# Performance work log

Hardware: AMD Instinct MI355X
Metric: run time of the kernel (lower is better)

Reference implementation:

```python
import jax, jax.numpy as jnp
import numpy as np

B, T, D, H, S = 512, 256, 128, 128, 32


def _param(key, shape, scale):
    return (jax.random.normal(key, shape, dtype=jnp.float32) * scale)


def setup_inputs() -> dict:
    key = jax.random.key(0)
    ks = jax.random.split(key, 32)
    sD = 1.0 / np.sqrt(D)
    sH = 1.0 / np.sqrt(H)
    inp = {
        'x': jax.random.normal(ks[0], (B, T, D), dtype=jnp.float32),
        'statics': jax.random.normal(ks[1], (B, S), dtype=jnp.float32),
        'mask': (jax.random.uniform(ks[2], (B, T, D)) > 0.5).astype(jnp.float32),
        'delta': jax.random.uniform(ks[3], (B, T, D), dtype=jnp.float32),
        'x_last_observed': jax.random.normal(ks[4], (B, T, D), dtype=jnp.float32),
        'x_mean': jax.random.normal(ks[5], (B, D), dtype=jnp.float32),
        'hs0': jax.random.normal(ks[6], (B, H), dtype=jnp.float32),
        # GRU-D decay params
        'w_dg_x': _param(ks[7], (D,), sD), 'b_dg_x': jnp.zeros((D,), jnp.float32),
        'W_dg_h': _param(ks[8], (H, D), sD), 'b_dg_h': jnp.zeros((H,), jnp.float32),
        # gates: update z, reset r, candidate h
        'W_z': _param(ks[9], (H, D), sD), 'U_z': _param(ks[10], (H, H), sH),
        'V_z': _param(ks[11], (H, D), sD), 'b_z': jnp.zeros((H,), jnp.float32),
        'W_r': _param(ks[12], (H, D), sD), 'U_r': _param(ks[13], (H, H), sH),
        'V_r': _param(ks[14], (H, D), sD), 'b_r': jnp.zeros((H,), jnp.float32),
        'W_h': _param(ks[15], (H, D), sD), 'U_h': _param(ks[16], (H, H), sH),
        'V_h': _param(ks[17], (H, D), sD), 'b_h': jnp.zeros((H,), jnp.float32),
        # classifier
        'W_out': _param(ks[18], (1, H + S), 1.0 / np.sqrt(H + S)),
        'b_out': jnp.zeros((1,), jnp.float32),
    }
    return inp


def reference(x, statics, mask, delta, x_last_observed, x_mean, hs0,
              w_dg_x, b_dg_x, W_dg_h, b_dg_h,
              W_z, U_z, V_z, b_z, W_r, U_r, V_r, b_r,
              W_h, U_h, V_h, b_h, W_out, b_out):
    # scan over time: inputs [T, B, D]
    xs = jnp.transpose(x, (1, 0, 2))
    ms = jnp.transpose(mask, (1, 0, 2))
    ds = jnp.transpose(delta, (1, 0, 2))
    xl = jnp.transpose(x_last_observed, (1, 0, 2))

    def step(h, inputs):
        xv, m, d, xlast = inputs
        gamma_x = jnp.exp(-jax.nn.relu(w_dg_x * d + b_dg_x))            # [B, D]
        gamma_h = jnp.exp(-jax.nn.relu(d @ W_dg_h.T + b_dg_h))          # [B, H]
        x_hat = m * xv + (1.0 - m) * (gamma_x * xlast + (1.0 - gamma_x) * x_mean)
        h = gamma_h * h
        z = jax.nn.sigmoid(x_hat @ W_z.T + h @ U_z.T + m @ V_z.T + b_z)
        r = jax.nn.sigmoid(x_hat @ W_r.T + h @ U_r.T + m @ V_r.T + b_r)
        h_tilde = jnp.tanh(x_hat @ W_h.T + (r * h) @ U_h.T + m @ V_h.T + b_h)
        h = (1.0 - z) * h + z * h_tilde
        return h, None

    h_final, _ = jax.lax.scan(step, hs0, (xs, ms, ds, xl))
    full = jnp.concatenate([h_final, statics], axis=1)                  # [B, H+S]
    predictions = full @ W_out.T + b_out                                # [B, 1]
    return predictions
```

## Files before the change

kernel.cpp:

```cpp
#include <hip/hip_runtime.h>
#include <stdint.h>


#define B_ 512
#define T_ 256
#define D_ 128
#define H_ 128
#define S_ 32
#define NE 512
#define KA 384
#define M_ (B_*T_)
#define HP 136
#define ESLAB ((size_t)NE * 16)
#define ESTRIDE ((size_t)32 * ESLAB)

typedef __attribute__((ext_vector_type(8))) short short8;
typedef __attribute__((ext_vector_type(4))) float f32x4;

#define BAR_LDS() asm volatile("s_waitcnt lgkmcnt(0)\n\ts_barrier" ::: "memory")

__device__ __forceinline__ unsigned short f2bf(float f) {
  union { float f; uint32_t u; } v; v.f = f;
  return (unsigned short)((v.u + 0x7FFFu + ((v.u >> 16) & 1u)) >> 16);
}
__device__ __forceinline__ unsigned short f2bf_fast(float f) {
  union { float f; uint32_t u; } v; v.f = f;
  return (unsigned short)((v.u + 0x8000u) >> 16);
}
__device__ __forceinline__ float bf2f(uint32_t s) {
  union { uint32_t u; float f; } v; v.u = s << 16;
  return v.f;
}

__device__ __forceinline__ uint2  ldraw(const unsigned short* p) { return *(const uint2*)p; }
__device__ __forceinline__ float4 ldraw(const float* p)          { return *(const float4*)p; }
__device__ __forceinline__ void unp(uint2 v, float o[4]) {
  o[0] = bf2f(v.x & 0xffffu); o[1] = bf2f(v.x >> 16);
  o[2] = bf2f(v.y & 0xffffu); o[3] = bf2f(v.y >> 16);
}
__device__ __forceinline__ void unp(float4 v, float o[4]) {
  o[0] = v.x; o[1] = v.y; o[2] = v.z; o[3] = v.w;
}
__device__ __forceinline__ void st4(unsigned short* p, const float v[4]) {
  uint2 u;
  u.x = (uint32_t)f2bf(v[0]) | ((uint32_t)f2bf(v[1]) << 16);
  u.y = (uint32_t)f2bf(v[2]) | ((uint32_t)f2bf(v[3]) << 16);
  *(uint2*)p = u;
}
__device__ __forceinline__ void st4(float* p, const float v[4]) {
  *(float4*)p = make_float4(v[0], v[1], v[2], v[3]);
}

__device__ __forceinline__ float fsigmoid(float x) {
  return __builtin_amdgcn_rcpf(1.f + __expf(-x));
}
__device__ __forceinline__ float ftanh(float x) {
  return 1.f - 2.f * __builtin_amdgcn_rcpf(1.f + __expf(2.f * x));
}

#define ASYNC_CP16(gsrc, ldst) \
  __builtin_amdgcn_global_load_lds((const __attribute__((address_space(1))) void*)(gsrc), \
                                   (__attribute__((address_space(3))) void*)(ldst), 16, 0, 0)

__global__ void prep_weights(const float* __restrict__ Wz, const float* __restrict__ Vz,
                             const float* __restrict__ Wr, const float* __restrict__ Vr,
                             const float* __restrict__ Wh, const float* __restrict__ Vh,
                             const float* __restrict__ Wdgh,
                             const float* __restrict__ bz, const float* __restrict__ br,
                             const float* __restrict__ bh, const float* __restrict__ bdgh,
                             unsigned short* __restrict__ Wcat, float* __restrict__ bias)
{
  int id = blockIdx.x * 256 + threadIdx.x;
  if (id < NE * KA) {
    int n = id / KA, k = id - n * KA;
    float v = 0.f;
    if (n < 384) {
      int nn = n & 127;
      const float* W = (n < 128) ? Wz : (n < 256) ? Wr : Wh;
      const float* V = (n < 128) ? Vz : (n < 256) ? Vr : Vh;
      if (k < 128)      v = W[nn * 128 + k];
      else if (k < 256) v = V[nn * 128 + (k - 128)];
    } else {
      if (k >= 256) v = Wdgh[(n - 384) * 128 + (k - 256)];
    }
    Wcat[id] = f2bf(v);
  }
  if (id < NE) {
    bias[id] = (id < 128) ? bz[id] : (id < 256) ? br[id - 128]
             : (id < 384) ? bh[id - 256] : bdgh[id - 384];
  }
}

__global__ void build_A(const float* __restrict__ x, const float* __restrict__ mask,
                        const float* __restrict__ delta, const float* __restrict__ xlast,
                        const float* __restrict__ xmean,
                        const float* __restrict__ wdgx, const float* __restrict__ bdgx,
                        unsigned short* __restrict__ Abuf)
{
  int id = blockIdx.x * 256 + threadIdx.x;
  int m = id >> 5;
  int c = id & 31;
  int t = m >> 9;
  int b = m & (B_ - 1);
  int k = c * 4;
  size_t src = ((size_t)b * T_ + t) * D_ + k;
  float4 xv = *(const float4*)(x + src);
  float4 mv = *(const float4*)(mask + src);
  float4 dv = *(const float4*)(delta + src);
  float4 lv = *(const float4*)(xlast + src);
  float4 uv = *(const float4*)(xmean + (size_t)b * D_ + k);
  float4 wv = *(const float4*)(wdgx + k);
  float4 bv = *(const float4*)(bdgx + k);
  const float* xp = (const float*)&xv; const float* mp = (const float*)&mv;
  const float* dp = (const float*)&dv; const float* lp = (const float*)&lv;
  const float* up = (const float*)&uv; const float* wp = (const float*)&wv;
  const float* bp = (const float*)&bv;
  unsigned short xh[4], mm[4], dd[4];
  #pragma unroll
  for (int i = 0; i < 4; ++i) {
    float g = __expf(-fmaxf(wp[i] * dp[i] + bp[i], 0.f));
    float xhat = mp[i] * xp[i] + (1.f - mp[i]) * (g * lp[i] + (1.f - g) * up[i]);
    xh[i] = f2bf(xhat); mm[i] = f2bf(mp[i]); dd[i] = f2bf(dp[i]);
  }
  uint2 px, pm, pd;
  px.x = (uint32_t)xh[0] | ((uint32_t)xh[1] << 16); px.y = (uint32_t)xh[2] | ((uint32_t)xh[3] << 16);
  pm.x = (uint32_t)mm[0] | ((uint32_t)mm[1] << 16); pm.y = (uint32_t)mm[2] | ((uint32_t)mm[3] << 16);
  pd.x = (uint32_t)dd[0] | ((uint32_t)dd[1] << 16); pd.y = (uint32_t)dd[2] | ((uint32_t)dd[3] << 16);
  unsigned short* rowp = Abuf + (size_t)m * KA;
  *(uint2*)(rowp + k)       = px;
  *(uint2*)(rowp + 128 + k) = pm;
  *(uint2*)(rowp + 256 + k) = pd;
}

template <typename ET>
__global__ __launch_bounds__(256, 2) void gemm_phase1(
    const unsigned short* __restrict__ Abuf, const unsigned short* __restrict__ Wcat,
    const float* __restrict__ bias, ET* __restrict__ E)
{
  __shared__ unsigned short As[3][4096];
  __shared__ unsigned short Bs[3][8192];
  const int tid = threadIdx.x;
  const int wave = tid >> 6, lane = tid & 63;
  const int q = lane >> 4, rl = lane & 15;
  const int m0 = blockIdx.x * 128;
  const int n0 = blockIdx.y * 256;
  const int wm = (wave >> 1) * 64, wn = (wave & 1) * 128;

  f32x4 acc[4][8];
  #pragma unroll
  for (int a = 0; a < 4; ++a)
    #pragma unroll
    for (int b = 0; b < 8; ++b) acc[a][b] = (f32x4){0.f, 0.f, 0.f, 0.f};

  #define STAGE(kt_) do {                                                     \
    const int kbase_ = (kt_) * 32; const int buf_ = (kt_) % 3;                \
    _Pragma("unroll")                                                         \
    for (int i = 0; i < 2; ++i) {                                             \
      int chunk = i * 256 + wave * 64 + lane;                                 \
      int row = chunk >> 2, kc = chunk & 3;                                   \
      ASYNC_CP16(Abuf + (size_t)(m0 + row) * KA + kbase_ + kc * 8,            \
                 &As[buf_][(i * 256 + wave * 64) * 8]);                       \
    }                                                                         \
    _Pragma("unroll")                                                         \
    for (int i = 0; i < 4; ++i) {                                             \
      int chunk = i * 256 + wave * 64 + lane;                                 \
      int row = chunk >> 2, kc = chunk & 3;                                   \
      ASYNC_CP16(Wcat + (size_t)(n0 + row) * KA + kbase_ + kc * 8,            \
                 &Bs[buf_][(i * 256 + wave * 64) * 8]);                       \
    }                                                                         \
  } while (0)

  STAGE(0);
  STAGE(1);

  #pragma unroll
  for (int kt = 0; kt < 12; ++kt) {
    if (kt == 11) asm volatile("s_waitcnt vmcnt(0)" ::: "memory");
    else          asm volatile("s_waitcnt vmcnt(6)" ::: "memory");
    asm volatile("s_barrier" ::: "memory");
    if (kt < 10) STAGE(kt + 2);
    const int buf = kt % 3;
    short8 af[4], bfr[8];
    #pragma unroll
    for (int tm = 0; tm < 4; ++tm)
      af[tm] = *(const short8*)(&As[buf][(wm + tm * 16 + rl) * 32 + q * 8]);
    #pragma unroll
    for (int tn = 0; tn < 8; ++tn)
      bfr[tn] = *(const short8*)(&Bs[buf][(wn + tn * 16 + rl) * 32 + q * 8]);
    #pragma unroll
    for (int tm = 0; tm < 4; ++tm)
      #pragma unroll
      for (int tn = 0; tn < 8; ++tn)
        acc[tm][tn] = __builtin_amdgcn_mfma_f32_16x16x32_bf16(af[tm], bfr[tn], acc[tm][tn], 0, 0, 0);
  }
  #undef STAGE

  const int t = m0 >> 9;
  const int bbase = m0 & (B_ - 1);
  #pragma unroll
  for (int tn = 0; tn < 8; ++tn) {
    int n = n0 + wn + tn * 16 + rl;
    float bv = bias[n];
    bool isg = (n >= 384);
    #pragma unroll
    for (int tm = 0; tm < 4; ++tm) {
      int brow = bbase + wm + tm * 16;
      float v[4];
      #pragma unroll
      for (int reg = 0; reg < 4; ++reg) {
        float xv = acc[tm][tn][reg] + bv;
        v[reg] = isg ? __expf(-fmaxf(xv, 0.f)) : xv;
      }
      st4(E + ((size_t)t * 32 + (brow >> 4)) * ESLAB + (size_t)n * 16 + q * 4, v);
    }
  }
}

template <typename ET>
__global__ __launch_bounds__(512, 2) void grud_scan(
    const ET* __restrict__ E,
    const float* __restrict__ Uz, const float* __restrict__ Ur, const float* __restrict__ Uh,
    const float* __restrict__ hs0, const float* __restrict__ statics,
    const float* __restrict__ Wout, const float* __restrict__ bout,
    float* __restrict__ out)
{
  __shared__ unsigned short hdec[16 * HP];
  __shared__ unsigned short rhb[16 * HP];
  __shared__ float hfin[16 * HP];
  const int tid = threadIdx.x;
  const int wave = tid >> 6, lane = tid & 63;
  const int q = lane >> 4, rl = lane & 15;
  const int col = wave * 16 + rl;
  const int b0 = blockIdx.x * 16;

  short8 uz[4], ur[4], uh[4];
  #pragma unroll
  for (int kc = 0; kc < 4; ++kc) {
    int koff = kc * 32 + q * 8;
    const float* pzw = Uz + col * H_ + koff;
    const float* prw = Ur + col * H_ + koff;
    const float* phw = Uh + col * H_ + koff;
    #pragma unroll
    for (int j = 0; j < 8; ++j) {
      uz[kc][j] = (short)f2bf(pzw[j]);
      ur[kc][j] = (short)f2bf(prw[j]);
      uh[kc][j] = (short)f2bf(phw[j]);
    }
  }

  const ET* pz = E + (size_t)blockIdx.x * ESLAB + (size_t)col * 16 + q * 4;
  const ET* pr = pz + 128 * 16;
  const ET* ph = pz + 256 * 16;
  const ET* pg = pz + 384 * 16;

  using RawT = decltype(ldraw((const ET*)nullptr));
  RawT cz, cr, chh, cg, nz{}, nr{}, nh{}, ng{};
  cz  = ldraw(pz);
  cr  = ldraw(pr);
  chh = ldraw(ph);
  cg  = ldraw(pg + ESTRIDE);
  RawT g0raw = ldraw(pg);

  float hd[4], g0[4];
  unp(g0raw, g0);
  #pragma unroll
  for (int reg = 0; reg < 4; ++reg) {
    int row = q * 4 + reg;
    float h0 = hs0[(b0 + row) * H_ + col];
    hd[reg] = g0[reg] * h0;
    hdec[row * HP + col] = f2bf_fast(hd[reg]);
  }
  BAR_LDS();

  for (int t = 0; t < T_; ++t) {
    if (t + 1 < T_) {
      size_t off = (size_t)(t + 1) * ESTRIDE;
      nz = ldraw(pz + off); nr = ldraw(pr + off); nh = ldraw(ph + off);
      if (t + 2 < T_) ng = ldraw(pg + (size_t)(t + 2) * ESTRIDE);
    }
    float Pz[4], Pr[4], Ph[4];
    unp(cz, Pz); unp(cr, Pr); unp(chh, Ph);

    short8 af[4];
    #pragma unroll
    for (int kc = 0; kc < 4; ++kc)
      af[kc] = *(const short8*)(&hdec[rl * HP + kc * 32 + q * 8]);
    f32x4 accz = (f32x4){0.f,0.f,0.f,0.f}, accr = (f32x4){0.f,0.f,0.f,0.f};
    #pragma unroll
    for (int kc = 0; kc < 4; ++kc) {
      accz = __builtin_amdgcn_mfma_f32_16x16x32_bf16(af[kc], uz[kc], accz, 0, 0, 0);
      accr = __builtin_amdgcn_mfma_f32_16x16x32_bf16(af[kc], ur[kc], accr, 0, 0, 0);
    }
    float zz[4];
    #pragma unroll
    for (int reg = 0; reg < 4; ++reg) {
      zz[reg] = fsigmoid(accz[reg] + Pz[reg]);
      float rr = fsigmoid(accr[reg] + Pr[reg]);
      rhb[(q * 4 + reg) * HP + col] = f2bf_fast(rr * hd[reg]);
    }
    BAR_LDS();

    short8 ar[4];
    #pragma unroll
    for (int kc = 0; kc < 4; ++kc)
      ar[kc] = *(const short8*)(&rhb[rl * HP + kc * 32 + q * 8]);
    f32x4 acch = (f32x4){0.f,0.f,0.f,0.f};
    #pragma unroll
    for (int kc = 0; kc < 4; ++kc)
      acch = __builtin_amdgcn_mfma_f32_16x16x32_bf16(ar[kc], uh[kc], acch, 0, 0, 0);

    if (t < T_ - 1) {
      float Gn[4];
      unp(cg, Gn);
      #pragma unroll
      for (int reg = 0; reg < 4; ++reg) {
        float ht = ftanh(acch[reg] + Ph[reg]);
        float hn = hd[reg] + zz[reg] * (ht - hd[reg]);
        hd[reg] = Gn[reg] * hn;
        hdec[(q * 4 + reg) * HP + col] = f2bf_fast(hd[reg]);
      }
    } else {
      #pragma unroll
      for (int reg = 0; reg < 4; ++reg) {
        float ht = ftanh(acch[reg] + Ph[reg]);
        float hn = hd[reg] + zz[reg] * (ht - hd[reg]);
        hfin[(q * 4 + reg) * HP + col] = hn;
      }
    }
    BAR_LDS();

    cz = nz; cr = nr; chh = nh; cg = ng;
  }

  {
    int row = tid >> 5, j = tid & 31;
    float acc = 0.f;
    #pragma unroll
    for (int c0 = 0; c0 < 4; ++c0)
      acc += hfin[row * HP + j + c0 * 32] * Wout[j + c0 * 32];
    acc += statics[(size_t)(b0 + row) * S_ + j] * Wout[H_ + j];
    #pragma unroll
    for (int off = 16; off >= 1; off >>= 1)
      acc += __shfl_down(acc, off, 32);
    if (j == 0) out[b0 + row] = acc + bout[0];
  }
}

template <typename ET>
static void launch_all(void* const* d_in, float* out, char* ws, hipStream_t stream)
{
  const float* x      = (const float*)d_in[0];
  const float* statics= (const float*)d_in[1];
  const float* mask   = (const float*)d_in[2];
  const float* delta  = (const float*)d_in[3];
  const float* xlast  = (const float*)d_in[4];
  const float* xmean  = (const float*)d_in[5];
  const float* hs0    = (const float*)d_in[6];
  const float* wdgx   = (const float*)d_in[7];
  const float* bdgx   = (const float*)d_in[8];
  const float* Wdgh   = (const float*)d_in[9];
  const float* bdgh   = (const float*)d_in[10];
  const float* Wz     = (const float*)d_in[11];
  const float* Uz     = (const float*)d_in[12];
  const float* Vz     = (const float*)d_in[13];
  const float* bz     = (const float*)d_in[14];
  const float* Wr     = (const float*)d_in[15];
  const float* Ur     = (const float*)d_in[16];
  const float* Vr     = (const float*)d_in[17];
  const float* br     = (const float*)d_in[18];
  const float* Wh     = (const float*)d_in[19];
  const float* Uh     = (const float*)d_in[20];
  const float* Vh     = (const float*)d_in[21];
  const float* bh     = (const float*)d_in[22];
  const float* Wout   = (const float*)d_in[23];
  const float* bout   = (const float*)d_in[24];

  const size_t eBytes = (size_t)M_ * NE * sizeof(ET);
  const size_t aBytes = (size_t)M_ * KA * 2;
  const size_t wBytes = (size_t)NE * KA * 2;
  ET* E = (ET*)ws;
  unsigned short* Abuf = (unsigned short*)(ws + eBytes);
  unsigned short* Wcat = (unsigned short*)(ws + eBytes + aBytes);
  float* bias = (float*)(ws + eBytes + aBytes + wBytes);

  prep_weights<<<768, 256, 0, stream>>>(Wz, Vz, Wr, Vr, Wh, Vh, Wdgh,
                                        bz, br, bh, bdgh, Wcat, bias);
  build_A<<<(M_ * 32) / 256, 256, 0, stream>>>(x, mask, delta, xlast, xmean,
                                               wdgx, bdgx, Abuf);
  gemm_phase1<ET><<<dim3(M_ / 128, NE / 256), 256, 0, stream>>>(Abuf, Wcat, bias, E);
  grud_scan<ET><<<B_ / 16, 512, 0, stream>>>(E, Uz, Ur, Uh, hs0, statics, Wout, bout, out);
}

extern "C" void kernel_launch(void* const* d_in, const int* in_sizes, int n_in,
                              void* d_out, int out_size, void* d_ws, size_t ws_size,
                              hipStream_t stream)
{
  char* ws = (char*)d_ws;
  float* out = (float*)d_out;
  const size_t common = (size_t)M_ * KA * 2 + (size_t)NE * KA * 2 + 8192;
  const size_t needF32 = (size_t)M_ * NE * 4 + common;
  const size_t needBF  = (size_t)M_ * NE * 2 + common;
  if (ws_size >= needF32)     launch_all<float>(d_in, out, ws, stream);
  else if (ws_size >= needBF) launch_all<unsigned short>(d_in, out, ws, stream);
}
```

Measured before the change: 574.2 us.

## Fuse input preprocessing into the phase-1 GEMM and widen block to all N

Removes the separate build_A kernel and its bf16 A buffer. The GEMM now loads x, mask, delta and x_last directly, computes x_hat and the bf16 conversion in registers, and writes the result to LDS. Each block now covers all 512 output columns with 512 threads, so the A tile is produced once per M tile instead of once per N split. The cost is that the pipeline drops from three stages to two and waits on vmcnt(0) at every step. The fp32 loads are also synchronous and sit on the critical path, and occupancy falls to one large block per CU.

```diff
diff --git a/kernel.cpp b/kernel.cpp
--- a/kernel.cpp
+++ b/kernel.cpp
@@ -91,60 +91,30 @@
   }
 }
 
-__global__ void build_A(const float* __restrict__ x, const float* __restrict__ mask,
-                        const float* __restrict__ delta, const float* __restrict__ xlast,
-                        const float* __restrict__ xmean,
-                        const float* __restrict__ wdgx, const float* __restrict__ bdgx,
-                        unsigned short* __restrict__ Abuf)
-{
-  int id = blockIdx.x * 256 + threadIdx.x;
-  int m = id >> 5;
-  int c = id & 31;
-  int t = m >> 9;
-  int b = m & (B_ - 1);
-  int k = c * 4;
-  size_t src = ((size_t)b * T_ + t) * D_ + k;
-  float4 xv = *(const float4*)(x + src);
-  float4 mv = *(const float4*)(mask + src);
-  float4 dv = *(const float4*)(delta + src);
-  float4 lv = *(const float4*)(xlast + src);
-  float4 uv = *(const float4*)(xmean + (size_t)b * D_ + k);
-  float4 wv = *(const float4*)(wdgx + k);
-  float4 bv = *(const float4*)(bdgx + k);
-  const float* xp = (const float*)&xv; const float* mp = (const float*)&mv;
-  const float* dp = (const float*)&dv; const float* lp = (const float*)&lv;
-  const float* up = (const float*)&uv; const float* wp = (const float*)&wv;
-  const float* bp = (const float*)&bv;
-  unsigned short xh[4], mm[4], dd[4];
-  #pragma unroll
-  for (int i = 0; i < 4; ++i) {
-    float g = __expf(-fmaxf(wp[i] * dp[i] + bp[i], 0.f));
-    float xhat = mp[i] * xp[i] + (1.f - mp[i]) * (g * lp[i] + (1.f - g) * up[i]);
-    xh[i] = f2bf(xhat); mm[i] = f2bf(mp[i]); dd[i] = f2bf(dp[i]);
-  }
-  uint2 px, pm, pd;
-  px.x = (uint32_t)xh[0] | ((uint32_t)xh[1] << 16); px.y = (uint32_t)xh[2] | ((uint32_t)xh[3] << 16);
-  pm.x = (uint32_t)mm[0] | ((uint32_t)mm[1] << 16); pm.y = (uint32_t)mm[2] | ((uint32_t)mm[3] << 16);
-  pd.x = (uint32_t)dd[0] | ((uint32_t)dd[1] << 16); pd.y = (uint32_t)dd[2] | ((uint32_t)dd[3] << 16);
-  unsigned short* rowp = Abuf + (size_t)m * KA;
-  *(uint2*)(rowp + k)       = px;
-  *(uint2*)(rowp + 128 + k) = pm;
-  *(uint2*)(rowp + 256 + k) = pd;
-}
-
 template <typename ET>
-__global__ __launch_bounds__(256, 2) void gemm_phase1(
-    const unsigned short* __restrict__ Abuf, const unsigned short* __restrict__ Wcat,
+__global__ __launch_bounds__(512, 1) void gemm_fused(
+    const float* __restrict__ x, const float* __restrict__ mask,
+    const float* __restrict__ delta, const float* __restrict__ xlast,
+    const float* __restrict__ xmean,
+    const float* __restrict__ wdgx, const float* __restrict__ bdgx,
+    const unsigned short* __restrict__ Wcat,
     const float* __restrict__ bias, ET* __restrict__ E)
 {
-  __shared__ unsigned short As[3][4096];
-  __shared__ unsigned short Bs[3][8192];
+  __shared__ unsigned short As[2][128 * 32];
+  __shared__ unsigned short Bs[2][512 * 32];
   const int tid = threadIdx.x;
   const int wave = tid >> 6, lane = tid & 63;
   const int q = lane >> 4, rl = lane & 15;
   const int m0 = blockIdx.x * 128;
-  const int n0 = blockIdx.y * 256;
-  const int wm = (wave >> 1) * 64, wn = (wave & 1) * 128;
+  const int t = m0 >> 9;
+  const int bbase = m0 & (B_ - 1);
+  const int wm = (wave >> 2) * 64;
+  const int wn = (wave & 3) * 128;
+
+  const int srow = tid >> 2;
+  const int kq = tid & 3;
+  const int b_g = bbase + srow;
+  const size_t xoff = ((size_t)b_g * T_ + t) * D_;
 
   f32x4 acc[4][8];
   #pragma unroll
@@ -152,54 +122,141 @@
     #pragma unroll
     for (int b = 0; b < 8; ++b) acc[a][b] = (f32x4){0.f, 0.f, 0.f, 0.f};
 
-  #define STAGE(kt_) do {                                                     \
-    const int kbase_ = (kt_) * 32; const int buf_ = (kt_) % 3;                \
-    _Pragma("unroll")                                                         \
-    for (int i = 0; i < 2; ++i) {                                             \
-      int chunk = i * 256 + wave * 64 + lane;                                 \
-      int row = chunk >> 2, kc = chunk & 3;                                   \
-      ASYNC_CP16(Abuf + (size_t)(m0 + row) * KA + kbase_ + kc * 8,            \
-                 &As[buf_][(i * 256 + wave * 64) * 8]);                       \
-    }                                                                         \
+  float4 sx0, sx1, sm0, sm1, sd0, sd1, sl0, sl1;
+
+  #define ISSUE_B(kt_, buf_) do {                                             \
     _Pragma("unroll")                                                         \
     for (int i = 0; i < 4; ++i) {                                             \
-      int chunk = i * 256 + wave * 64 + lane;                                 \
+      int chunk = i * 512 + wave * 64 + lane;                                 \
       int row = chunk >> 2, kc = chunk & 3;                                   \
-      ASYNC_CP16(Wcat + (size_t)(n0 + row) * KA + kbase_ + kc * 8,            \
-                 &Bs[buf_][(i * 256 + wave * 64) * 8]);                       \
+      ASYNC_CP16(Wcat + (size_t)row * KA + (kt_) * 32 + kc * 8,               \
+                 &Bs[buf_][(i * 512 + wave * 64) * 8]);                       \
     }                                                                         \
   } while (0)
 
-  STAGE(0);
-  STAGE(1);
+  #define ISSUE_A(kt_) do {                                                   \
+    if ((kt_) < 4) {                                                          \
+      int d0 = (kt_) * 32 + kq * 8;                                           \
+      sx0 = *(const float4*)(x + xoff + d0);                                  \
+      sx1 = *(const float4*)(x + xoff + d0 + 4);                              \
+      sm0 = *(const float4*)(mask + xoff + d0);                               \
+      sm1 = *(const float4*)(mask + xoff + d0 + 4);                           \
+      sd0 = *(const float4*)(delta + xoff + d0);                              \
+      sd1 = *(const float4*)(delta + xoff + d0 + 4);                          \
+      sl0 = *(const float4*)(xlast + xoff + d0);                              \
+      sl1 = *(const float4*)(xlast + xoff + d0 + 4);                          \
+    } else if ((kt_) < 8) {                                                   \
+      int d0 = ((kt_) - 4) * 32 + kq * 8;                                     \
+      sm0 = *(const float4*)(mask + xoff + d0);                               \
+      sm1 = *(const float4*)(mask + xoff + d0 + 4);                           \
+    } else {                                                                  \
+      int d0 = ((kt_) - 8) * 32 + kq * 8;                                     \
+      sd0 = *(const float4*)(delta + xoff + d0);                              \
+      sd1 = *(const float4*)(delta + xoff + d0 + 4);                          \
+    }                                                                         \
+  } while (0)
+
+  #define CONVERT_A(kt_, buf_) do {                                           \
+    short8 ov;                                                                \
+    if ((kt_) < 4) {                                                          \
+      int d0 = (kt_) * 32 + kq * 8;                                           \
+      float U[8], W[8], C[8], X[8], Mm[8], Dd[8], L[8];                       \
+      *(float4*)&U[0] = *(const float4*)(xmean + (size_t)b_g * D_ + d0);      \
+      *(float4*)&U[4] = *(const float4*)(xmean + (size_t)b_g * D_ + d0 + 4);  \
+      *(float4*)&W[0] = *(const float4*)(wdgx + d0);                          \
+      *(float4*)&W[4] = *(const float4*)(wdgx + d0 + 4);                      \
+      *(float4*)&C[0] = *(const float4*)(bdgx + d0);                          \
+      *(float4*)&C[4] = *(const float4*)(bdgx + d0 + 4);                      \
+      *(float4*)&X[0] = sx0; *(float4*)&X[4] = sx1;                           \
+      *(float4*)&Mm[0] = sm0; *(float4*)&Mm[4] = sm1;                         \
+      *(float4*)&Dd[0] = sd0; *(float4*)&Dd[4] = sd1;                         \
+      *(float4*)&L[0] = sl0; *(float4*)&L[4] = sl1;                           \
+      _Pragma("unroll")                                                       \
+      for (int i = 0; i < 8; ++i) {                                           \
+        float g = __expf(-fmaxf(W[i] * Dd[i] + C[i], 0.f));                   \
+        float xh = Mm[i] * X[i] + (1.f - Mm[i]) * (g * L[i] + (1.f - g) * U[i]); \
+        ov[i] = (short)f2bf(xh);                                              \
+      }                                                                       \
+    } else if ((kt_) < 8) {                                                   \
+      float Mm[8];                                                            \
+      *(float4*)&Mm[0] = sm0; *(float4*)&Mm[4] = sm1;                         \
+      _Pragma("unroll")                                                       \
+      for (int i = 0; i < 8; ++i) ov[i] = (short)f2bf(Mm[i]);                 \
+    } else {                                                                  \
+      float Dd[8];                                                            \
+      *(float4*)&Dd[0] = sd0; *(float4*)&Dd[4] = sd1;                         \
+      _Pragma("unroll")                                                       \
+      for (int i = 0; i < 8; ++i) ov[i] = (short)f2bf(Dd[i]);                 \
+    }                                                                         \
+    *(short8*)(&As[buf_][srow * 32 + kq * 8]) = ov;                           \
+  } while (0)
+
+  ISSUE_A(0); ISSUE_B(0, 0);
+  asm volatile("s_waitcnt vmcnt(0)" ::: "memory");
+  CONVERT_A(0, 0);
+  BAR_LDS();
+  ISSUE_A(1); ISSUE_B(1, 1);
 
   #pragma unroll
   for (int kt = 0; kt < 12; ++kt) {
-    if (kt == 11) asm volatile("s_waitcnt vmcnt(0)" ::: "memory");
-    else          asm volatile("s_waitcnt vmcnt(6)" ::: "memory");
-    asm volatile("s_barrier" ::: "memory");
-    if (kt < 10) STAGE(kt + 2);
-    const int buf = kt % 3;
+    const int cur = kt & 1;
     short8 af[4], bfr[8];
     #pragma unroll
     for (int tm = 0; tm < 4; ++tm)
-      af[tm] = *(const short8*)(&As[buf][(wm + tm * 16 + rl) * 32 + q * 8]);
+      af[tm] = *(const short8*)(&As[cur][(wm + tm * 16 + rl) * 32 + q * 8]);
     #pragma unroll
     for (int tn = 0; tn < 8; ++tn)
-      bfr[tn] = *(const short8*)(&Bs[buf][(wn + tn * 16 + rl) * 32 + q * 8]);
+      bfr[tn] = *(const short8*)(&Bs[cur][(wn + tn * 16 + rl) * 32 + q * 8]);
     #pragma unroll
     for (int tm = 0; tm < 4; ++tm)
       #pragma unroll
       for (int tn = 0; tn < 8; ++tn)
         acc[tm][tn] = __builtin_amdgcn_mfma_f32_16x16x32_bf16(af[tm], bfr[tn], acc[tm][tn], 0, 0, 0);
-  }
-  #undef STAGE
-
-  const int t = m0 >> 9;
-  const int bbase = m0 & (B_ - 1);
+    if (kt < 11) {
+      asm volatile("s_waitcnt vmcnt(0)" ::: "memory");
+      if (kt == 0)      CONVERT_A(1, 1);
+      else if (kt == 1) CONVERT_A(2, 0);
+      else if (kt == 2) CONVERT_A(3, 1);
+      else if (kt == 3) CONVERT_A(4, 0);
+      else if (kt == 4) CONVERT_A(5, 1);
+      else if (kt == 5) CONVERT_A(6, 0);
+      else if (kt == 6) CONVERT_A(7, 1);
+      else if (kt == 7) CONVERT_A(8, 0);
+      else if (kt == 8) CONVERT_A(9, 1);
+      else if (kt == 9) CONVERT_A(10, 0);
+      else              CONVERT_A(11, 1);
+      BAR_LDS();
+      if (kt < 10) {
+        if (kt == 0)      { ISSUE_A(2); }
+        else if (kt == 1) { ISSUE_A(3); }
+        else if (kt == 2) { ISSUE_A(4); }
+        else if (kt == 3) { ISSUE_A(5); }
+        else if (kt == 4) { ISSUE_A(6); }
+        else if (kt == 5) { ISSUE_A(7); }
+        else if (kt == 6) { ISSUE_A(8); }
+        else if (kt == 7) { ISSUE_A(9); }
+        else if (kt == 8) { ISSUE_A(10); }
+        else              { ISSUE_A(11); }
+        if (kt == 0)      ISSUE_B(2, 0);
+        else if (kt == 1) ISSUE_B(3, 1);
+        else if (kt == 2) ISSUE_B(4, 0);
+        else if (kt == 3) ISSUE_B(5, 1);
+        else if (kt == 4) ISSUE_B(6, 0);
+        else if (kt == 5) ISSUE_B(7, 1);
+        else if (kt == 6) ISSUE_B(8, 0);
+        else if (kt == 7) ISSUE_B(9, 1);
+        else if (kt == 8) ISSUE_B(10, 0);
+        else              ISSUE_B(11, 1);
+      }
+    }
+  }
+  #undef ISSUE_A
+  #undef ISSUE_B
+  #undef CONVERT_A
+
   #pragma unroll
   for (int tn = 0; tn < 8; ++tn) {
-    int n = n0 + wn + tn * 16 + rl;
+    int n = wn + tn * 16 + rl;
     float bv = bias[n];
     bool isg = (n >= 384);
     #pragma unroll
@@ -376,18 +433,15 @@
   const float* bout   = (const float*)d_in[24];
 
   const size_t eBytes = (size_t)M_ * NE * sizeof(ET);
-  const size_t aBytes = (size_t)M_ * KA * 2;
   const size_t wBytes = (size_t)NE * KA * 2;
   ET* E = (ET*)ws;
-  unsigned short* Abuf = (unsigned short*)(ws + eBytes);
-  unsigned short* Wcat = (unsigned short*)(ws + eBytes + aBytes);
-  float* bias = (float*)(ws + eBytes + aBytes + wBytes);
+  unsigned short* Wcat = (unsigned short*)(ws + eBytes);
+  float* bias = (float*)(ws + eBytes + wBytes);
 
   prep_weights<<<768, 256, 0, stream>>>(Wz, Vz, Wr, Vr, Wh, Vh, Wdgh,
                                         bz, br, bh, bdgh, Wcat, bias);
-  build_A<<<(M_ * 32) / 256, 256, 0, stream>>>(x, mask, delta, xlast, xmean,
-                                               wdgx, bdgx, Abuf);
-  gemm_phase1<ET><<<dim3(M_ / 128, NE / 256), 256, 0, stream>>>(Abuf, Wcat, bias, E);
+  gemm_fused<ET><<<M_ / 128, 512, 0, stream>>>(x, mask, delta, xlast, xmean,
+                                               wdgx, bdgx, Wcat, bias, E);
   grud_scan<ET><<<B_ / 16, 512, 0, stream>>>(E, Uz, Ur, Uh, hs0, statics, Wout, bout, out);
 }
 
@@ -397,7 +451,7 @@
 {
   char* ws = (char*)d_ws;
   float* out = (float*)d_out;
-  const size_t common = (size_t)M_ * KA * 2 + (size_t)NE * KA * 2 + 8192;
+  const size_t common = (size_t)NE * KA * 2 + 8192;
   const size_t needF32 = (size_t)M_ * NE * 4 + common;
   const size_t needBF  = (size_t)M_ * NE * 2 + common;
   if (ws_size >= needF32)     launch_all<float>(d_in, out, ws, stream);
```

Measured after the change: 681.6 us. 1.19x slower.

## Always store gate pre-activations in bf16 and restructure build_A per batch row

Applied to the files above, without the earlier changes.

Drops the fp32 intermediate path, so the big E buffer of gate pre-activations is always written and read as bf16, halving its memory traffic between the GEMM and the scan. build_A now runs one block per batch row and loops over time, reading the inputs contiguously and writing Abuf with nontemporal stores. The bf16 intermediate adds rounding error to the recurrence compared with the fp32 path, which was previously chosen whenever the workspace was large enough.

```diff
diff --git a/kernel.cpp b/kernel.cpp
--- a/kernel.cpp
+++ b/kernel.cpp
@@ -32,23 +32,16 @@
   return v.f;
 }
 
-__device__ __forceinline__ uint2  ldraw(const unsigned short* p) { return *(const uint2*)p; }
-__device__ __forceinline__ float4 ldraw(const float* p)          { return *(const float4*)p; }
+__device__ __forceinline__ uint2 ldraw(const unsigned short* p) { return *(const uint2*)p; }
 __device__ __forceinline__ void unp(uint2 v, float o[4]) {
   o[0] = bf2f(v.x & 0xffffu); o[1] = bf2f(v.x >> 16);
   o[2] = bf2f(v.y & 0xffffu); o[3] = bf2f(v.y >> 16);
-}
-__device__ __forceinline__ void unp(float4 v, float o[4]) {
-  o[0] = v.x; o[1] = v.y; o[2] = v.z; o[3] = v.w;
 }
 __device__ __forceinline__ void st4(unsigned short* p, const float v[4]) {
   uint2 u;
   u.x = (uint32_t)f2bf(v[0]) | ((uint32_t)f2bf(v[1]) << 16);
   u.y = (uint32_t)f2bf(v[2]) | ((uint32_t)f2bf(v[3]) << 16);
   *(uint2*)p = u;
-}
-__device__ __forceinline__ void st4(float* p, const float v[4]) {
-  *(float4*)p = make_float4(v[0], v[1], v[2], v[3]);
 }
 
 __device__ __forceinline__ float fsigmoid(float x) {
@@ -91,51 +84,56 @@
   }
 }
 
-__global__ void build_A(const float* __restrict__ x, const float* __restrict__ mask,
-                        const float* __restrict__ delta, const float* __restrict__ xlast,
-                        const float* __restrict__ xmean,
-                        const float* __restrict__ wdgx, const float* __restrict__ bdgx,
-                        unsigned short* __restrict__ Abuf)
-{
-  int id = blockIdx.x * 256 + threadIdx.x;
-  int m = id >> 5;
-  int c = id & 31;
-  int t = m >> 9;
-  int b = m & (B_ - 1);
-  int k = c * 4;
-  size_t src = ((size_t)b * T_ + t) * D_ + k;
-  float4 xv = *(const float4*)(x + src);
-  float4 mv = *(const float4*)(mask + src);
-  float4 dv = *(const float4*)(delta + src);
-  float4 lv = *(const float4*)(xlast + src);
-  float4 uv = *(const float4*)(xmean + (size_t)b * D_ + k);
-  float4 wv = *(const float4*)(wdgx + k);
-  float4 bv = *(const float4*)(bdgx + k);
-  const float* xp = (const float*)&xv; const float* mp = (const float*)&mv;
-  const float* dp = (const float*)&dv; const float* lp = (const float*)&lv;
-  const float* up = (const float*)&uv; const float* wp = (const float*)&wv;
-  const float* bp = (const float*)&bv;
-  unsigned short xh[4], mm[4], dd[4];
-  #pragma unroll
-  for (int i = 0; i < 4; ++i) {
-    float g = __expf(-fmaxf(wp[i] * dp[i] + bp[i], 0.f));
-    float xhat = mp[i] * xp[i] + (1.f - mp[i]) * (g * lp[i] + (1.f - g) * up[i]);
-    xh[i] = f2bf(xhat); mm[i] = f2bf(mp[i]); dd[i] = f2bf(dp[i]);
-  }
-  uint2 px, pm, pd;
-  px.x = (uint32_t)xh[0] | ((uint32_t)xh[1] << 16); px.y = (uint32_t)xh[2] | ((uint32_t)xh[3] << 16);
-  pm.x = (uint32_t)mm[0] | ((uint32_t)mm[1] << 16); pm.y = (uint32_t)mm[2] | ((uint32_t)mm[3] << 16);
-  pd.x = (uint32_t)dd[0] | ((uint32_t)dd[1] << 16); pd.y = (uint32_t)dd[2] | ((uint32_t)dd[3] << 16);
-  unsigned short* rowp = Abuf + (size_t)m * KA;
-  *(uint2*)(rowp + k)       = px;
-  *(uint2*)(rowp + 128 + k) = pm;
-  *(uint2*)(rowp + 256 + k) = pd;
-}
-
-template <typename ET>
+__global__ __launch_bounds__(256, 4) void build_A(
+    const float* __restrict__ x, const float* __restrict__ mask,
+    const float* __restrict__ delta, const float* __restrict__ xlast,
+    const float* __restrict__ xmean,
+    const float* __restrict__ wdgx, const float* __restrict__ bdgx,
+    unsigned short* __restrict__ Abuf)
+{
+  const int b = blockIdx.x;
+  const int dq = (threadIdx.x & 31) * 4;
+  const int tof = threadIdx.x >> 5;
+  const float4 wv = *(const float4*)(wdgx + dq);
+  const float4 cv = *(const float4*)(bdgx + dq);
+  const float4 uv = *(const float4*)(xmean + (size_t)b * D_ + dq);
+  const float* wp = (const float*)&wv;
+  const float* cp = (const float*)&cv;
+  const float* up = (const float*)&uv;
+  const size_t base = (size_t)b * T_ * D_;
+
+  for (int it = 0; it < T_ / 8; ++it) {
+    const int t = it * 8 + tof;
+    const size_t src = base + (size_t)t * D_ + dq;
+    float4 xv = *(const float4*)(x + src);
+    float4 mv = *(const float4*)(mask + src);
+    float4 dv = *(const float4*)(delta + src);
+    float4 lv = *(const float4*)(xlast + src);
+    const float* xp = (const float*)&xv; const float* mp = (const float*)&mv;
+    const float* dp = (const float*)&dv; const float* lp = (const float*)&lv;
+    unsigned short xh[4], mm[4], dd[4];
+    #pragma unroll
+    for (int i = 0; i < 4; ++i) {
+      float g = __expf(-fmaxf(wp[i] * dp[i] + cp[i], 0.f));
+      float xhat = mp[i] * xp[i] + (1.f - mp[i]) * (g * lp[i] + (1.f - g) * up[i]);
+      xh[i] = f2bf(xhat); mm[i] = f2bf(mp[i]); dd[i] = f2bf(dp[i]);
+    }
+    unsigned long long px = (unsigned long long)xh[0] | ((unsigned long long)xh[1] << 16)
+                          | ((unsigned long long)xh[2] << 32) | ((unsigned long long)xh[3] << 48);
+    unsigned long long pm = (unsigned long long)mm[0] | ((unsigned long long)mm[1] << 16)
+                          | ((unsigned long long)mm[2] << 32) | ((unsigned long long)mm[3] << 48);
+    unsigned long long pd = (unsigned long long)dd[0] | ((unsigned long long)dd[1] << 16)
+                          | ((unsigned long long)dd[2] << 32) | ((unsigned long long)dd[3] << 48);
+    unsigned short* rowp = Abuf + (size_t)(t * B_ + b) * KA;
+    __builtin_nontemporal_store(px, (unsigned long long*)(rowp + dq));
+    __builtin_nontemporal_store(pm, (unsigned long long*)(rowp + 128 + dq));
+    __builtin_nontemporal_store(pd, (unsigned long long*)(rowp + 256 + dq));
+  }
+}
+
 __global__ __launch_bounds__(256, 2) void gemm_phase1(
     const unsigned short* __restrict__ Abuf, const unsigned short* __restrict__ Wcat,
-    const float* __restrict__ bias, ET* __restrict__ E)
+    const float* __restrict__ bias, unsigned short* __restrict__ E)
 {
   __shared__ unsigned short As[3][4096];
   __shared__ unsigned short Bs[3][8192];
@@ -216,9 +214,8 @@
   }
 }
 
-template <typename ET>
 __global__ __launch_bounds__(512, 2) void grud_scan(
-    const ET* __restrict__ E,
+    const unsigned short* __restrict__ E,
     const float* __restrict__ Uz, const float* __restrict__ Ur, const float* __restrict__ Uh,
     const float* __restrict__ hs0, const float* __restrict__ statics,
     const float* __restrict__ Wout, const float* __restrict__ bout,
@@ -248,18 +245,17 @@
     }
   }
 
-  const ET* pz = E + (size_t)blockIdx.x * ESLAB + (size_t)col * 16 + q * 4;
-  const ET* pr = pz + 128 * 16;
-  const ET* ph = pz + 256 * 16;
-  const ET* pg = pz + 384 * 16;
-
-  using RawT = decltype(ldraw((const ET*)nullptr));
-  RawT cz, cr, chh, cg, nz{}, nr{}, nh{}, ng{};
+  const unsigned short* pz = E + (size_t)blockIdx.x * ESLAB + (size_t)col * 16 + q * 4;
+  const unsigned short* pr = pz + 128 * 16;
+  const unsigned short* ph = pz + 256 * 16;
+  const unsigned short* pg = pz + 384 * 16;
+
+  uint2 cz, cr, chh, cg, nz{}, nr{}, nh{}, ng{};
   cz  = ldraw(pz);
   cr  = ldraw(pr);
   chh = ldraw(ph);
   cg  = ldraw(pg + ESTRIDE);
-  RawT g0raw = ldraw(pg);
+  uint2 g0raw = ldraw(pg);
 
   float hd[4], g0[4];
   unp(g0raw, g0);
@@ -346,7 +342,6 @@
   }
 }
 
-template <typename ET>
 static void launch_all(void* const* d_in, float* out, char* ws, hipStream_t stream)
 {
   const float* x      = (const float*)d_in[0];
@@ -375,20 +370,20 @@
   const float* Wout   = (const float*)d_in[23];
   const float* bout   = (const float*)d_in[24];
 
-  const size_t eBytes = (size_t)M_ * NE * sizeof(ET);
+  const size_t eBytes = (size_t)M_ * NE * 2;
   const size_t aBytes = (size_t)M_ * KA * 2;
   const size_t wBytes = (size_t)NE * KA * 2;
-  ET* E = (ET*)ws;
+  unsigned short* E = (unsigned short*)ws;
   unsigned short* Abuf = (unsigned short*)(ws + eBytes);
   unsigned short* Wcat = (unsigned short*)(ws + eBytes + aBytes);
   float* bias = (float*)(ws + eBytes + aBytes + wBytes);
 
   prep_weights<<<768, 256, 0, stream>>>(Wz, Vz, Wr, Vr, Wh, Vh, Wdgh,
                                         bz, br, bh, bdgh, Wcat, bias);
-  build_A<<<(M_ * 32) / 256, 256, 0, stream>>>(x, mask, delta, xlast, xmean,
-                                               wdgx, bdgx, Abuf);
-  gemm_phase1<ET><<<dim3(M_ / 128, NE / 256), 256, 0, stream>>>(Abuf, Wcat, bias, E);
-  grud_scan<ET><<<B_ / 16, 512, 0, stream>>>(E, Uz, Ur, Uh, hs0, statics, Wout, bout, out);
+  build_A<<<B_, 256, 0, stream>>>(x, mask, delta, xlast, xmean,
+                                  wdgx, bdgx, Abuf);
+  gemm_phase1<<<dim3(M_ / 128, NE / 256), 256, 0, stream>>>(Abuf, Wcat, bias, E);
+  grud_scan<<<B_ / 16, 512, 0, stream>>>(E, Uz, Ur, Uh, hs0, statics, Wout, bout, out);
 }
 
 extern "C" void kernel_launch(void* const* d_in, const int* in_sizes, int n_in,
@@ -397,9 +392,7 @@
 {
   char* ws = (char*)d_ws;
   float* out = (float*)d_out;
-  const size_t common = (size_t)M_ * KA * 2 + (size_t)NE * KA * 2 + 8192;
-  const size_t needF32 = (size_t)M_ * NE * 4 + common;
-  const size_t needBF  = (size_t)M_ * NE * 2 + common;
-  if (ws_size >= needF32)     launch_all<float>(d_in, out, ws, stream);
-  else if (ws_size >= needBF) launch_all<unsigned short>(d_in, out, ws, stream);
-}
+  const size_t needBF = (size_t)M_ * NE * 2 + (size_t)M_ * KA * 2
+                      + (size_t)NE * KA * 2 + 8192;
+  if (ws_size >= needBF) launch_all(d_in, out, ws, stream);
+}
```

After: 583.9 us. No clear change (+1.7%).
